# Performance work log

Measured on AMD Instinct MI355X. Metric: run time of the kernel, lower is better.

The kernel has to match this reference:

```python
import jax, jax.numpy as jnp
import numpy as np

B, C, H, W = 8, 256, 128, 128


def setup_inputs() -> dict:
    key = jax.random.key(0)
    ks = jax.random.split(key, 4)
    scale = 1.0 / np.sqrt(C)
    x = jax.random.normal(ks[0], (B, C, H, W), dtype=jnp.float32)
    Wq = jax.random.normal(ks[1], (C, C), dtype=jnp.float32) * scale
    Wk = jax.random.normal(ks[2], (C, C), dtype=jnp.float32) * scale
    Wv = jax.random.normal(ks[3], (C, C), dtype=jnp.float32) * scale
    bq = jnp.zeros((C,), dtype=jnp.float32)
    bk = jnp.zeros((C,), dtype=jnp.float32)
    bv = jnp.zeros((C,), dtype=jnp.float32)
    gamma = jnp.zeros((1,), dtype=jnp.float32)
    return {"x": x, "Wq": Wq, "bq": bq, "Wk": Wk, "bk": bk, "Wv": Wv, "bv": bv, "gamma": gamma}


def reference(x, Wq, bq, Wk, bk, Wv, bv, gamma):
    b, c, h, w = x.shape
    n = h * w
    xf = x.reshape(b, c, n)  # [B, C, N]
    # 1x1 convs == per-pixel linear over channels (W is [out, in])
    q = jnp.einsum('bcn,oc->bon', xf, Wq) + bq[None, :, None]  # [B, C, N]
    k = jnp.einsum('bcn,oc->bon', xf, Wk) + bk[None, :, None]
    v = jnp.einsum('bcn,oc->bon', xf, Wv) + bv[None, :, None]
    # energy[b,i,j] = sum_n k[b,i,n] * q[b,j,n]  -> [B, C, C]
    energy = jnp.einsum('bin,bjn->bij', k, q)
    attention = jax.nn.softmax(energy, axis=-1)
    # out[b,j,n] = sum_i attention[b,i,j] * v[b,i,n]  (attention^T @ v)
    out = jnp.einsum('bij,bin->bjn', attention, v)
    out = out.reshape(b, c, h, w)
    return gamma[0] * out + x
```

## Files before the change

kernel.cpp:

```cpp
#include <hip/hip_runtime.h>

#define C_DIM 256
#define N_DIM 16384
#define NBATCH 8

typedef __bf16 bf16x4 __attribute__((ext_vector_type(4)));
typedef __bf16 bf16x8 __attribute__((ext_vector_type(8)));
typedef float  f32x4  __attribute__((ext_vector_type(4)));

#define OFF_G   0x000000u
#define OFF_SP  0x200000u
#define OFF_EK  0x240000u
#define OFF_EQ  0x242000u
#define OFF_D   0x244000u
#define OFF_T1  0x250000u
#define OFF_E   0x450000u
#define OFF_P   0x650000u
#define OFF_GP  0x1000000u

__device__ __forceinline__ unsigned sw_off(int row, int kbyte) {
  return (unsigned)(row * 128 + (kbyte ^ ((((row >> 2) ^ row) & 7) << 4)));
}
__device__ __forceinline__ float f4g(const float4& v, int i) {
  return reinterpret_cast<const float*>(&v)[i];
}

__global__ __launch_bounds__(512, 2) void k1_syrk(const float* __restrict__ x,
                                                  __bf16* __restrict__ Gp,
                                                  float* __restrict__ sp,
                                                  const float* __restrict__ gm) {
  if (gm[0] == 0.0f) return;
  __shared__ __align__(16) char Alds[256 * 128];
  __shared__ float s_lds[256];
  const int b = blockIdx.y;
  const float* xb = x + (size_t)b * C_DIM * N_DIM;
  const int tid = threadIdx.x, lane = tid & 63, wave = tid >> 6;
  const int wm = wave >> 1, wn = wave & 1;
  const int k4 = tid & 15, rowt = tid >> 4;
  const size_t nbase = (size_t)blockIdx.x * 512;
  f32x4 acc[4][8] = {};
  float spart[8];
#pragma unroll
  for (int p = 0; p < 8; ++p) spart[p] = 0.f;

  float4 va[8];
  {
#pragma unroll
    for (int p = 0; p < 8; ++p)
      va[p] = *(const float4*)&xb[(size_t)(rowt + p * 32) * N_DIM + nbase + 4 * k4];
  }

  for (int ks = 0; ks < 8; ++ks) {
    __syncthreads();
#pragma unroll
    for (int p = 0; p < 8; ++p) {
      const int row = rowt + p * 32;
      spart[p] += va[p].x + va[p].y + va[p].z + va[p].w;
      bf16x4 ha = { (__bf16)va[p].x, (__bf16)va[p].y, (__bf16)va[p].z, (__bf16)va[p].w };
      *(bf16x4*)(Alds + sw_off(row, 8 * k4)) = ha;
    }
    __syncthreads();
    if (ks < 7) {
      const size_t n0 = nbase + (size_t)(ks + 1) * 64 + 4 * k4;
#pragma unroll
      for (int p = 0; p < 8; ++p)
        va[p] = *(const float4*)&xb[(size_t)(rowt + p * 32) * N_DIM + n0];
    }
#pragma unroll
    for (int kk = 0; kk < 2; ++kk) {
      bf16x8 af[4], bfr[8];
      const int kbyte = (kk * 32 + (lane >> 4) * 8) * 2;
#pragma unroll
      for (int mi = 0; mi < 4; ++mi)
        af[mi] = *(const bf16x8*)(Alds + sw_off(wm * 64 + mi * 16 + (lane & 15), kbyte));
#pragma unroll
      for (int ni = 0; ni < 8; ++ni)
        bfr[ni] = *(const bf16x8*)(Alds + sw_off(wn * 128 + ni * 16 + (lane & 15), kbyte));
#pragma unroll
      for (int mi = 0; mi < 4; ++mi)
#pragma unroll
        for (int ni = 0; ni < 8; ++ni)
          acc[mi][ni] = __builtin_amdgcn_mfma_f32_16x16x32_bf16(af[mi], bfr[ni], acc[mi][ni], 0, 0, 0);
    }
  }

  __bf16* Gout = Gp + ((size_t)blockIdx.x * NBATCH + b) * 65536;
#pragma unroll
  for (int mi = 0; mi < 4; ++mi)
#pragma unroll
    for (int ni = 0; ni < 8; ++ni)
#pragma unroll
      for (int r = 0; r < 4; ++r) {
        const int gr = wm * 64 + mi * 16 + (lane >> 4) * 4 + r;
        const int gc = wn * 128 + ni * 16 + (lane & 15);
        Gout[gr * 256 + gc] = (__bf16)acc[mi][ni][r];
      }

  __syncthreads();
  if (tid < 256) s_lds[tid] = 0.f;
  __syncthreads();
#pragma unroll
  for (int p = 0; p < 8; ++p) atomicAdd(&s_lds[rowt + p * 32], spart[p]);
  __syncthreads();
  if (tid < 256) sp[((size_t)blockIdx.x * NBATCH + b) * 256 + tid] = s_lds[tid];
}

__global__ __launch_bounds__(256) void k1_reduce(const __bf16* __restrict__ Gp,
                                                 float* __restrict__ G,
                                                 const float* __restrict__ Wq,
                                                 const float* __restrict__ Wk,
                                                 const float* __restrict__ sp,
                                                 float* __restrict__ ek,
                                                 float* __restrict__ eq,
                                                 const float* __restrict__ gm) {
  if (gm[0] == 0.0f) return;
  if (blockIdx.x >= 256) {
    __shared__ float s_sh[256];
    const int b = blockIdx.x - 256;
    const int t = threadIdx.x;
    float sv = 0.f;
#pragma unroll
    for (int p = 0; p < 32; ++p) sv += sp[((size_t)p * NBATCH + b) * 256 + t];
    s_sh[t] = sv;
    __syncthreads();
    float aK = 0.f, aQ = 0.f;
#pragma unroll 8
    for (int i = 0; i < 256; i += 4) {
      const float4 wk4 = *(const float4*)&Wk[t * 256 + i];
      const float4 wq4 = *(const float4*)&Wq[t * 256 + i];
      const float4 svv = *(const float4*)&s_sh[i];
      aK += wk4.x * svv.x + wk4.y * svv.y + wk4.z * svv.z + wk4.w * svv.w;
      aQ += wq4.x * svv.x + wq4.y * svv.y + wq4.z * svv.z + wq4.w * svv.w;
    }
    ek[b * 256 + t] = aK;
    eq[b * 256 + t] = aQ;
    return;
  }
  const size_t idx = ((size_t)blockIdx.x * 256 + threadIdx.x) * 8;
  float acc[8] = {};
#pragma unroll
  for (int p = 0; p < 32; ++p) {
    const bf16x8 v = *(const bf16x8*)&Gp[(size_t)p * NBATCH * 65536 + idx];
#pragma unroll
    for (int j = 0; j < 8; ++j) acc[j] += (float)v[j];
  }
  f32x4 lo = { acc[0], acc[1], acc[2], acc[3] };
  f32x4 hi = { acc[4], acc[5], acc[6], acc[7] };
  *(f32x4*)&G[idx]     = lo;
  *(f32x4*)&G[idx + 4] = hi;
}

__global__ __launch_bounds__(256) void k2_nt(const float* __restrict__ Ag, int abatch,
                                             const float* __restrict__ Bg, int bbatch,
                                             float* __restrict__ Cg,
                                             const float* __restrict__ ek,
                                             const float* __restrict__ bq,
                                             const float* __restrict__ bk,
                                             const float* __restrict__ eq,
                                             float Nf, int bias,
                                             const float* __restrict__ gm) {
  if (gm[0] == 0.0f) return;
  const int b = blockIdx.z;
  const float* A = Ag + (abatch ? (size_t)b * 65536 : 0);
  const float* B = Bg + (bbatch ? (size_t)b * 65536 : 0);
  float* Cb = Cg + (size_t)b * 65536;
  const int i0 = blockIdx.y * 64 + 4 * (threadIdx.x >> 4);
  const int c0 = blockIdx.x * 64 + 4 * (threadIdx.x & 15);
  float acc[4][4] = {};
  for (int k = 0; k < 256; k += 4) {
    float4 av[4], bv4[4];
#pragma unroll
    for (int r = 0; r < 4; ++r) av[r] = *(const float4*)&A[(size_t)(i0 + r) * 256 + k];
#pragma unroll
    for (int s2 = 0; s2 < 4; ++s2) bv4[s2] = *(const float4*)&B[(size_t)(c0 + s2) * 256 + k];
#pragma unroll
    for (int r = 0; r < 4; ++r)
#pragma unroll
      for (int s2 = 0; s2 < 4; ++s2)
        acc[r][s2] += av[r].x * bv4[s2].x + av[r].y * bv4[s2].y +
                      av[r].z * bv4[s2].z + av[r].w * bv4[s2].w;
  }
#pragma unroll
  for (int r = 0; r < 4; ++r)
#pragma unroll
    for (int s2 = 0; s2 < 4; ++s2) {
      const int i = i0 + r, j = c0 + s2;
      float v = acc[r][s2];
      if (bias) v += ek[b * 256 + i] * bq[j] + bk[i] * (eq[b * 256 + j] + Nf * bq[j]);
      Cb[(size_t)i * 256 + j] = v;
    }
}

__global__ __launch_bounds__(256) void k2_softmax(float* __restrict__ E,
                                                  const float* __restrict__ gm) {
  if (gm[0] == 0.0f) return;
  const int gw = blockIdx.x * 4 + (threadIdx.x >> 6);
  const int b = gw >> 8, i = gw & 255;
  const int lane = threadIdx.x & 63;
  float* row = E + (size_t)b * 65536 + (size_t)i * 256;
  float4 v = *(const float4*)&row[lane * 4];
  float m = fmaxf(fmaxf(v.x, v.y), fmaxf(v.z, v.w));
  for (int o = 32; o > 0; o >>= 1) m = fmaxf(m, __shfl_xor(m, o));
  v.x = __expf(v.x - m); v.y = __expf(v.y - m);
  v.z = __expf(v.z - m); v.w = __expf(v.w - m);
  float sum = v.x + v.y + v.z + v.w;
  for (int o = 32; o > 0; o >>= 1) sum += __shfl_xor(sum, o);
  const float inv = 1.0f / sum;
  v.x *= inv; v.y *= inv; v.z *= inv; v.w *= inv;
  *(float4*)&row[lane * 4] = v;
}

__global__ __launch_bounds__(256) void k2_pprime(const float* __restrict__ Att,
                                                 const float* __restrict__ Wv,
                                                 const float* __restrict__ bv,
                                                 const float* __restrict__ gm,
                                                 __bf16* __restrict__ P,
                                                 float* __restrict__ dv) {
  if (gm[0] == 0.0f) return;
  const int b = blockIdx.z;
  const float* Ab = Att + (size_t)b * 65536;
  const int j0 = blockIdx.y * 64 + 4 * (threadIdx.x >> 4);
  const int c0 = blockIdx.x * 64 + 4 * (threadIdx.x & 15);
  float acc[4][4] = {};
#pragma unroll 4
  for (int i = 0; i < 256; ++i) {
    float4 av = *(const float4*)&Ab[(size_t)i * 256 + j0];
    float4 wv = *(const float4*)&Wv[(size_t)i * 256 + c0];
#pragma unroll
    for (int r = 0; r < 4; ++r) {
      const float a = f4g(av, r);
#pragma unroll
      for (int s2 = 0; s2 < 4; ++s2) acc[r][s2] += a * f4g(wv, s2);
    }
  }
  const float g = gm[0];
  __bf16* Pb = P + (size_t)b * 65536;
#pragma unroll
  for (int r = 0; r < 4; ++r)
#pragma unroll
    for (int s2 = 0; s2 < 4; ++s2) {
      const float v = g * acc[r][s2] + ((j0 + r) == (c0 + s2) ? 1.f : 0.f);
      Pb[(size_t)(j0 + r) * 256 + c0 + s2] = (__bf16)v;
    }
  if (blockIdx.x == 0 && threadIdx.x < 64) {
    const int j = blockIdx.y * 64 + threadIdx.x;
    float a = 0.f;
    for (int i = 0; i < 256; ++i) a += Ab[(size_t)i * 256 + j] * bv[i];
    dv[b * 256 + j] = g * a;
  }
}

__global__ __launch_bounds__(512) void k3_out(const float* __restrict__ x,
                                              const __bf16* __restrict__ P,
                                              const float* __restrict__ dvec,
                                              const float* __restrict__ gm,
                                              float* __restrict__ out) {
  const int b = blockIdx.y, nt = blockIdx.x;
  const float* xb = x + (size_t)b * C_DIM * N_DIM;
  float* ob = out + (size_t)b * C_DIM * N_DIM;
  const int tid = threadIdx.x;
  const int n0 = nt * 128;

  if (gm[0] == 0.0f) {
#pragma unroll
    for (int it = 0; it < 16; ++it) {
      const int idx = it * 512 + tid;
      const int row = idx >> 5;
      const int c4  = (idx & 31) * 4;
      *(float4*)&ob[(size_t)row * N_DIM + n0 + c4] =
          *(const float4*)&xb[(size_t)row * N_DIM + n0 + c4];
    }
    return;
  }

  __shared__ __align__(16) char Alds[256 * 128];
  __shared__ __align__(16) char Blds[128 * 128];
  const __bf16* Pb = P + (size_t)b * 65536;
  const int lane = tid & 63, wave = tid >> 6;
  const int jw = wave >> 1, nw = wave & 1;
  const int k4 = tid & 15, rowt = tid >> 4;
  const int nq = tid & 31, cq = tid >> 5;
  f32x4 acc[4][4] = {};

  bf16x4 pa[8];
  float4 xv[4];
  {
#pragma unroll
    for (int p = 0; p < 8; ++p)
      pa[p] = *(const bf16x4*)&Pb[(size_t)(rowt + p * 32) * 256 + 4 * k4];
    const int cc = 4 * cq;
#pragma unroll
    for (int r = 0; r < 4; ++r)
      xv[r] = *(const float4*)&xb[(size_t)(cc + r) * N_DIM + n0 + 4 * nq];
  }

  for (int ks = 0; ks < 4; ++ks) {
    __syncthreads();
#pragma unroll
    for (int p = 0; p < 8; ++p)
      *(bf16x4*)(Alds + sw_off(rowt + p * 32, 8 * k4)) = pa[p];
    {
      const int cb = (4 * cq) * 2;
#pragma unroll
      for (int i = 0; i < 4; ++i) {
        bf16x4 t = { (__bf16)f4g(xv[0], i), (__bf16)f4g(xv[1], i),
                     (__bf16)f4g(xv[2], i), (__bf16)f4g(xv[3], i) };
        *(bf16x4*)(Blds + sw_off(4 * nq + i, cb)) = t;
      }
    }
    __syncthreads();
    if (ks < 3) {
      const int c0 = (ks + 1) * 64;
#pragma unroll
      for (int p = 0; p < 8; ++p)
        pa[p] = *(const bf16x4*)&Pb[(size_t)(rowt + p * 32) * 256 + c0 + 4 * k4];
      const int cc = c0 + 4 * cq;
#pragma unroll
      for (int r = 0; r < 4; ++r)
        xv[r] = *(const float4*)&xb[(size_t)(cc + r) * N_DIM + n0 + 4 * nq];
    }
#pragma unroll
    for (int kk = 0; kk < 2; ++kk) {
      bf16x8 af[4], bfr[4];
      const int kbyte = (kk * 32 + (lane >> 4) * 8) * 2;
#pragma unroll
      for (int mi = 0; mi < 4; ++mi)
        af[mi] = *(const bf16x8*)(Alds + sw_off(jw * 64 + mi * 16 + (lane & 15), kbyte));
#pragma unroll
      for (int ni = 0; ni < 4; ++ni)
        bfr[ni] = *(const bf16x8*)(Blds + sw_off(nw * 64 + ni * 16 + (lane & 15), kbyte));
#pragma unroll
      for (int mi = 0; mi < 4; ++mi)
#pragma unroll
        for (int ni = 0; ni < 4; ++ni)
          acc[mi][ni] = __builtin_amdgcn_mfma_f32_16x16x32_bf16(af[mi], bfr[ni], acc[mi][ni], 0, 0, 0);
    }
  }

#pragma unroll
  for (int mi = 0; mi < 4; ++mi)
#pragma unroll
    for (int ni = 0; ni < 4; ++ni)
#pragma unroll
      for (int r = 0; r < 4; ++r) {
        const int j = jw * 64 + mi * 16 + (lane >> 4) * 4 + r;
        const int n = n0 + nw * 64 + ni * 16 + (lane & 15);
        ob[(size_t)j * N_DIM + n] = acc[mi][ni][r] + dvec[b * 256 + j];
      }
}

extern "C" void kernel_launch(void* const* d_in, const int* in_sizes, int n_in,
                              void* d_out, int out_size, void* d_ws, size_t ws_size,
                              hipStream_t stream) {
  const float* x  = (const float*)d_in[0];
  const float* Wq = (const float*)d_in[1];
  const float* bq = (const float*)d_in[2];
  const float* Wk = (const float*)d_in[3];
  const float* bk = (const float*)d_in[4];
  const float* Wv = (const float*)d_in[5];
  const float* bv = (const float*)d_in[6];
  const float* gm = (const float*)d_in[7];
  float* out = (float*)d_out;
  char* ws = (char*)d_ws;
  float* G  = (float*)(ws + OFF_G);
  float* sp = (float*)(ws + OFF_SP);
  float* ek = (float*)(ws + OFF_EK);
  float* eq = (float*)(ws + OFF_EQ);
  float* dv = (float*)(ws + OFF_D);
  float* T1 = (float*)(ws + OFF_T1);
  float* E  = (float*)(ws + OFF_E);
  __bf16* P = (__bf16*)(ws + OFF_P);
  __bf16* Gp = (__bf16*)(ws + OFF_GP);


  k1_syrk<<<dim3(32, 8), dim3(512), 0, stream>>>(x, Gp, sp, gm);
  k1_reduce<<<dim3(264), dim3(256), 0, stream>>>(Gp, G, Wq, Wk, sp, ek, eq, gm);
  k2_nt<<<dim3(4, 4, 8), dim3(256), 0, stream>>>(Wk, 0, G, 1, T1,
                                                 nullptr, nullptr, nullptr, nullptr, 0.f, 0, gm);
  k2_nt<<<dim3(4, 4, 8), dim3(256), 0, stream>>>(T1, 1, Wq, 0, E,
                                                 ek, bq, bk, eq, (float)N_DIM, 1, gm);
  k2_softmax<<<dim3(512), dim3(256), 0, stream>>>(E, gm);
  k2_pprime<<<dim3(4, 4, 8), dim3(256), 0, stream>>>(E, Wv, bv, gm, P, dv);
  k3_out<<<dim3(128, 8), dim3(512), 0, stream>>>(x, P, dv, gm, out);
}
```

Measured before the change: 57.88 us.

## Fuse middle attention kernels into one per-batch kernel; streamline gamma-zero copy

Replaces the reduce, two small GEMMs, softmax and P-prime kernels with a single kernel that runs one 512-thread block per batch. Energy, softmax and projection now run in sequence inside that block, with workspace round-trips and block-wide syncs between stages. The intent is to cut kernel launches and inter-kernel gaps, since these stages exit early when gamma is zero. The gamma-zero path of the output kernel now copies contiguous flat chunks with nontemporal stores. The trade-off is that with nonzero gamma the fused middle stage runs on only 8 blocks, so it has far less parallelism.

```diff
diff --git a/kernel.cpp b/kernel.cpp
--- a/kernel.cpp
+++ b/kernel.cpp
@@ -8,10 +8,7 @@
 typedef __bf16 bf16x8 __attribute__((ext_vector_type(8)));
 typedef float  f32x4  __attribute__((ext_vector_type(4)));
 
-#define OFF_G   0x000000u
 #define OFF_SP  0x200000u
-#define OFF_EK  0x240000u
-#define OFF_EQ  0x242000u
 #define OFF_D   0x244000u
 #define OFF_T1  0x250000u
 #define OFF_E   0x450000u
@@ -105,148 +102,160 @@
   if (tid < 256) sp[((size_t)blockIdx.x * NBATCH + b) * 256 + tid] = s_lds[tid];
 }
 
-__global__ __launch_bounds__(256) void k1_reduce(const __bf16* __restrict__ Gp,
-                                                 float* __restrict__ G,
-                                                 const float* __restrict__ Wq,
-                                                 const float* __restrict__ Wk,
-                                                 const float* __restrict__ sp,
-                                                 float* __restrict__ ek,
-                                                 float* __restrict__ eq,
-                                                 const float* __restrict__ gm) {
-  if (gm[0] == 0.0f) return;
-  if (blockIdx.x >= 256) {
-    __shared__ float s_sh[256];
-    const int b = blockIdx.x - 256;
-    const int t = threadIdx.x;
-    float sv = 0.f;
-#pragma unroll
-    for (int p = 0; p < 32; ++p) sv += sp[((size_t)p * NBATCH + b) * 256 + t];
-    s_sh[t] = sv;
-    __syncthreads();
-    float aK = 0.f, aQ = 0.f;
-#pragma unroll 8
-    for (int i = 0; i < 256; i += 4) {
-      const float4 wk4 = *(const float4*)&Wk[t * 256 + i];
-      const float4 wq4 = *(const float4*)&Wq[t * 256 + i];
-      const float4 svv = *(const float4*)&s_sh[i];
-      aK += wk4.x * svv.x + wk4.y * svv.y + wk4.z * svv.z + wk4.w * svv.w;
-      aQ += wq4.x * svv.x + wq4.y * svv.y + wq4.z * svv.z + wq4.w * svv.w;
-    }
-    ek[b * 256 + t] = aK;
-    eq[b * 256 + t] = aQ;
-    return;
-  }
-  const size_t idx = ((size_t)blockIdx.x * 256 + threadIdx.x) * 8;
-  float acc[8] = {};
-#pragma unroll
-  for (int p = 0; p < 32; ++p) {
-    const bf16x8 v = *(const bf16x8*)&Gp[(size_t)p * NBATCH * 65536 + idx];
-#pragma unroll
-    for (int j = 0; j < 8; ++j) acc[j] += (float)v[j];
-  }
-  f32x4 lo = { acc[0], acc[1], acc[2], acc[3] };
-  f32x4 hi = { acc[4], acc[5], acc[6], acc[7] };
-  *(f32x4*)&G[idx]     = lo;
-  *(f32x4*)&G[idx + 4] = hi;
-}
-
-__global__ __launch_bounds__(256) void k2_nt(const float* __restrict__ Ag, int abatch,
-                                             const float* __restrict__ Bg, int bbatch,
-                                             float* __restrict__ Cg,
-                                             const float* __restrict__ ek,
+__global__ __launch_bounds__(512) void k_mid(const __bf16* __restrict__ Gp,
+                                             const float* __restrict__ Wq,
+                                             const float* __restrict__ Wk,
+                                             const float* __restrict__ Wv,
+                                             const float* __restrict__ sp,
                                              const float* __restrict__ bq,
                                              const float* __restrict__ bk,
-                                             const float* __restrict__ eq,
-                                             float Nf, int bias,
-                                             const float* __restrict__ gm) {
+                                             const float* __restrict__ bv,
+                                             const float* __restrict__ gm,
+                                             float* __restrict__ Gbuf,
+                                             float* __restrict__ T1buf,
+                                             __bf16* __restrict__ P,
+                                             float* __restrict__ dv) {
   if (gm[0] == 0.0f) return;
-  const int b = blockIdx.z;
-  const float* A = Ag + (abatch ? (size_t)b * 65536 : 0);
-  const float* B = Bg + (bbatch ? (size_t)b * 65536 : 0);
-  float* Cb = Cg + (size_t)b * 65536;
-  const int i0 = blockIdx.y * 64 + 4 * (threadIdx.x >> 4);
-  const int c0 = blockIdx.x * 64 + 4 * (threadIdx.x & 15);
-  float acc[4][4] = {};
-  for (int k = 0; k < 256; k += 4) {
-    float4 av[4], bv4[4];
-#pragma unroll
-    for (int r = 0; r < 4; ++r) av[r] = *(const float4*)&A[(size_t)(i0 + r) * 256 + k];
-#pragma unroll
-    for (int s2 = 0; s2 < 4; ++s2) bv4[s2] = *(const float4*)&B[(size_t)(c0 + s2) * 256 + k];
-#pragma unroll
-    for (int r = 0; r < 4; ++r)
-#pragma unroll
-      for (int s2 = 0; s2 < 4; ++s2)
-        acc[r][s2] += av[r].x * bv4[s2].x + av[r].y * bv4[s2].y +
-                      av[r].z * bv4[s2].z + av[r].w * bv4[s2].w;
-  }
-#pragma unroll
-  for (int r = 0; r < 4; ++r)
-#pragma unroll
-    for (int s2 = 0; s2 < 4; ++s2) {
-      const int i = i0 + r, j = c0 + s2;
-      float v = acc[r][s2];
-      if (bias) v += ek[b * 256 + i] * bq[j] + bk[i] * (eq[b * 256 + j] + Nf * bq[j]);
-      Cb[(size_t)i * 256 + j] = v;
-    }
-}
-
-__global__ __launch_bounds__(256) void k2_softmax(float* __restrict__ E,
-                                                  const float* __restrict__ gm) {
-  if (gm[0] == 0.0f) return;
-  const int gw = blockIdx.x * 4 + (threadIdx.x >> 6);
-  const int b = gw >> 8, i = gw & 255;
-  const int lane = threadIdx.x & 63;
-  float* row = E + (size_t)b * 65536 + (size_t)i * 256;
-  float4 v = *(const float4*)&row[lane * 4];
-  float m = fmaxf(fmaxf(v.x, v.y), fmaxf(v.z, v.w));
-  for (int o = 32; o > 0; o >>= 1) m = fmaxf(m, __shfl_xor(m, o));
-  v.x = __expf(v.x - m); v.y = __expf(v.y - m);
-  v.z = __expf(v.z - m); v.w = __expf(v.w - m);
-  float sum = v.x + v.y + v.z + v.w;
-  for (int o = 32; o > 0; o >>= 1) sum += __shfl_xor(sum, o);
-  const float inv = 1.0f / sum;
-  v.x *= inv; v.y *= inv; v.z *= inv; v.w *= inv;
-  *(float4*)&row[lane * 4] = v;
-}
-
-__global__ __launch_bounds__(256) void k2_pprime(const float* __restrict__ Att,
-                                                 const float* __restrict__ Wv,
-                                                 const float* __restrict__ bv,
-                                                 const float* __restrict__ gm,
-                                                 __bf16* __restrict__ P,
-                                                 float* __restrict__ dv) {
-  if (gm[0] == 0.0f) return;
-  const int b = blockIdx.z;
-  const float* Ab = Att + (size_t)b * 65536;
-  const int j0 = blockIdx.y * 64 + 4 * (threadIdx.x >> 4);
-  const int c0 = blockIdx.x * 64 + 4 * (threadIdx.x & 15);
-  float acc[4][4] = {};
-#pragma unroll 4
-  for (int i = 0; i < 256; ++i) {
-    float4 av = *(const float4*)&Ab[(size_t)i * 256 + j0];
-    float4 wv = *(const float4*)&Wv[(size_t)i * 256 + c0];
-#pragma unroll
-    for (int r = 0; r < 4; ++r) {
-      const float a = f4g(av, r);
-#pragma unroll
-      for (int s2 = 0; s2 < 4; ++s2) acc[r][s2] += a * f4g(wv, s2);
-    }
-  }
+  const int b = blockIdx.x, tid = threadIdx.x;
+  __shared__ float s_sh[256], ek_sh[256], eq_sh[256];
+  float* Gb  = Gbuf  + (size_t)b * 65536;
+  float* T1b = T1buf + (size_t)b * 65536;
+
+  if (tid < 256) {
+    float sv = 0.f;
+    for (int p = 0; p < 32; ++p) sv += sp[(size_t)(p * NBATCH + b) * 256 + tid];
+    s_sh[tid] = sv;
+  }
+  __syncthreads();
+  {
+    const int t = tid & 255;
+    const float* W = (tid < 256) ? Wk : Wq;
+    float a = 0.f;
+    for (int i = 0; i < 256; i += 4) {
+      const float4 w4 = *(const float4*)&W[(size_t)t * 256 + i];
+      const float4 s4 = *(const float4*)&s_sh[i];
+      a += w4.x * s4.x + w4.y * s4.y + w4.z * s4.z + w4.w * s4.w;
+    }
+    if (tid < 256) ek_sh[t] = a; else eq_sh[t] = a;
+  }
+
+  for (int u = 0; u < 16; ++u) {
+    const int c8 = (u * 512 + tid) * 8;
+    float acc[8] = {};
+    for (int p = 0; p < 32; ++p) {
+      const bf16x8 v = *(const bf16x8*)&Gp[(size_t)(p * NBATCH + b) * 65536 + c8];
+#pragma unroll
+      for (int j = 0; j < 8; ++j) acc[j] += (float)v[j];
+    }
+    f32x4 lo = { acc[0], acc[1], acc[2], acc[3] };
+    f32x4 hi = { acc[4], acc[5], acc[6], acc[7] };
+    *(f32x4*)&Gb[c8] = lo; *(f32x4*)&Gb[c8 + 4] = hi;
+  }
+  __syncthreads();
+
+  const int jv = 4 * (tid & 15);
+  const int iv = 4 * (tid >> 4);
+
+  for (int ib = 0; ib < 2; ++ib)
+    for (int jb = 0; jb < 4; ++jb) {
+      const int i0 = ib * 128 + iv, j0 = jb * 64 + jv;
+      float acc[4][4] = {};
+      for (int k = 0; k < 256; k += 4) {
+        float4 a4[4], g4[4];
+#pragma unroll
+        for (int r = 0; r < 4; ++r) a4[r] = *(const float4*)&Wk[(size_t)(i0 + r) * 256 + k];
+#pragma unroll
+        for (int kk = 0; kk < 4; ++kk) g4[kk] = *(const float4*)&Gb[(size_t)(k + kk) * 256 + j0];
+#pragma unroll
+        for (int r = 0; r < 4; ++r)
+#pragma unroll
+          for (int kk = 0; kk < 4; ++kk) {
+            const float av = f4g(a4[r], kk);
+#pragma unroll
+            for (int c = 0; c < 4; ++c) acc[r][c] += av * f4g(g4[kk], c);
+          }
+      }
+#pragma unroll
+      for (int r = 0; r < 4; ++r) {
+        f32x4 o = { acc[r][0], acc[r][1], acc[r][2], acc[r][3] };
+        *(f32x4*)&T1b[(size_t)(i0 + r) * 256 + j0] = o;
+      }
+    }
+  __syncthreads();
+
+  const float Nf = (float)N_DIM;
+  for (int ib = 0; ib < 2; ++ib)
+    for (int jb = 0; jb < 4; ++jb) {
+      const int i0 = ib * 128 + iv, j0 = jb * 64 + jv;
+      float acc[4][4] = {};
+      for (int k = 0; k < 256; k += 4) {
+        float4 a4[4], w4[4];
+#pragma unroll
+        for (int r = 0; r < 4; ++r) a4[r] = *(const float4*)&T1b[(size_t)(i0 + r) * 256 + k];
+#pragma unroll
+        for (int c = 0; c < 4; ++c) w4[c] = *(const float4*)&Wq[(size_t)(j0 + c) * 256 + k];
+#pragma unroll
+        for (int r = 0; r < 4; ++r)
+#pragma unroll
+          for (int c = 0; c < 4; ++c)
+            acc[r][c] += f4g(a4[r],0) * f4g(w4[c],0) + f4g(a4[r],1) * f4g(w4[c],1)
+                       + f4g(a4[r],2) * f4g(w4[c],2) + f4g(a4[r],3) * f4g(w4[c],3);
+      }
+#pragma unroll
+      for (int r = 0; r < 4; ++r)
+#pragma unroll
+        for (int c = 0; c < 4; ++c) {
+          const int i = i0 + r, j = j0 + c;
+          Gb[(size_t)i * 256 + j] = acc[r][c] + ek_sh[i] * bq[j] + bk[i] * (eq_sh[j] + Nf * bq[j]);
+        }
+    }
+  __syncthreads();
+
+  {
+    const int wv2 = tid >> 6, lane = tid & 63;
+    for (int rr = 0; rr < 32; ++rr) {
+      const int row = wv2 * 32 + rr;
+      float4 v = *(const float4*)&Gb[(size_t)row * 256 + lane * 4];
+      float m = fmaxf(fmaxf(v.x, v.y), fmaxf(v.z, v.w));
+      for (int o = 32; o > 0; o >>= 1) m = fmaxf(m, __shfl_xor(m, o));
+      v.x = __expf(v.x - m); v.y = __expf(v.y - m);
+      v.z = __expf(v.z - m); v.w = __expf(v.w - m);
+      float sum = v.x + v.y + v.z + v.w;
+      for (int o = 32; o > 0; o >>= 1) sum += __shfl_xor(sum, o);
+      const float inv = 1.0f / sum;
+      v.x *= inv; v.y *= inv; v.z *= inv; v.w *= inv;
+      *(float4*)&Gb[(size_t)row * 256 + lane * 4] = v;
+    }
+  }
+  __syncthreads();
+
   const float g = gm[0];
   __bf16* Pb = P + (size_t)b * 65536;
-#pragma unroll
-  for (int r = 0; r < 4; ++r)
-#pragma unroll
-    for (int s2 = 0; s2 < 4; ++s2) {
-      const float v = g * acc[r][s2] + ((j0 + r) == (c0 + s2) ? 1.f : 0.f);
-      Pb[(size_t)(j0 + r) * 256 + c0 + s2] = (__bf16)v;
-    }
-  if (blockIdx.x == 0 && threadIdx.x < 64) {
-    const int j = blockIdx.y * 64 + threadIdx.x;
+  for (int jb = 0; jb < 2; ++jb)
+    for (int cb = 0; cb < 4; ++cb) {
+      const int j0 = jb * 128 + iv, c0 = cb * 64 + jv;
+      float acc[4][4] = {};
+      for (int i = 0; i < 256; ++i) {
+        const float4 av  = *(const float4*)&Gb[(size_t)i * 256 + j0];
+        const float4 wv4 = *(const float4*)&Wv[(size_t)i * 256 + c0];
+#pragma unroll
+        for (int r = 0; r < 4; ++r) {
+          const float a = f4g(av, r);
+#pragma unroll
+          for (int c = 0; c < 4; ++c) acc[r][c] += a * f4g(wv4, c);
+        }
+      }
+#pragma unroll
+      for (int r = 0; r < 4; ++r)
+#pragma unroll
+        for (int c = 0; c < 4; ++c)
+          Pb[(size_t)(j0 + r) * 256 + c0 + c] =
+              (__bf16)(g * acc[r][c] + ((j0 + r) == (c0 + c) ? 1.f : 0.f));
+    }
+  if (tid < 256) {
     float a = 0.f;
-    for (int i = 0; i < 256; ++i) a += Ab[(size_t)i * 256 + j] * bv[i];
-    dv[b * 256 + j] = g * a;
+    for (int i = 0; i < 256; ++i) a += Gb[(size_t)i * 256 + tid] * bv[i];
+    dv[b * 256 + tid] = g * a;
   }
 }
 
@@ -255,31 +264,32 @@
                                               const float* __restrict__ dvec,
                                               const float* __restrict__ gm,
                                               float* __restrict__ out) {
+  const int tid = threadIdx.x;
+
+  if (gm[0] == 0.0f) {
+    const size_t base = (size_t)(blockIdx.y * gridDim.x + blockIdx.x) * 8192;
+    const f32x4* xi = (const f32x4*)x;
+    f32x4* oo = (f32x4*)out;
+#pragma unroll
+    for (int it = 0; it < 16; ++it) {
+      const size_t idx = base + (size_t)it * 512 + tid;
+      const f32x4 v = xi[idx];
+      __builtin_nontemporal_store(v, &oo[idx]);
+    }
+    return;
+  }
+
+  __shared__ __align__(16) char Alds[256 * 128];
+  __shared__ __align__(16) char Blds[128 * 128];
   const int b = blockIdx.y, nt = blockIdx.x;
   const float* xb = x + (size_t)b * C_DIM * N_DIM;
   float* ob = out + (size_t)b * C_DIM * N_DIM;
-  const int tid = threadIdx.x;
-  const int n0 = nt * 128;
-
-  if (gm[0] == 0.0f) {
-#pragma unroll
-    for (int it = 0; it < 16; ++it) {
-      const int idx = it * 512 + tid;
-      const int row = idx >> 5;
-      const int c4  = (idx & 31) * 4;
-      *(float4*)&ob[(size_t)row * N_DIM + n0 + c4] =
-          *(const float4*)&xb[(size_t)row * N_DIM + n0 + c4];
-    }
-    return;
-  }
-
-  __shared__ __align__(16) char Alds[256 * 128];
-  __shared__ __align__(16) char Blds[128 * 128];
   const __bf16* Pb = P + (size_t)b * 65536;
   const int lane = tid & 63, wave = tid >> 6;
   const int jw = wave >> 1, nw = wave & 1;
   const int k4 = tid & 15, rowt = tid >> 4;
   const int nq = tid & 31, cq = tid >> 5;
+  const int n0 = nt * 128;
   f32x4 acc[4][4] = {};
 
   bf16x4 pa[8];
@@ -362,24 +372,15 @@
   const float* gm = (const float*)d_in[7];
   float* out = (float*)d_out;
   char* ws = (char*)d_ws;
-  float* G  = (float*)(ws + OFF_G);
   float* sp = (float*)(ws + OFF_SP);
-  float* ek = (float*)(ws + OFF_EK);
-  float* eq = (float*)(ws + OFF_EQ);
   float* dv = (float*)(ws + OFF_D);
   float* T1 = (float*)(ws + OFF_T1);
-  float* E  = (float*)(ws + OFF_E);
+  float* Gb = (float*)(ws + OFF_E);
   __bf16* P = (__bf16*)(ws + OFF_P);
   __bf16* Gp = (__bf16*)(ws + OFF_GP);
 
-
   k1_syrk<<<dim3(32, 8), dim3(512), 0, stream>>>(x, Gp, sp, gm);
-  k1_reduce<<<dim3(264), dim3(256), 0, stream>>>(Gp, G, Wq, Wk, sp, ek, eq, gm);
-  k2_nt<<<dim3(4, 4, 8), dim3(256), 0, stream>>>(Wk, 0, G, 1, T1,
-                                                 nullptr, nullptr, nullptr, nullptr, 0.f, 0, gm);
-  k2_nt<<<dim3(4, 4, 8), dim3(256), 0, stream>>>(T1, 1, Wq, 0, E,
-                                                 ek, bq, bk, eq, (float)N_DIM, 1, gm);
-  k2_softmax<<<dim3(512), dim3(256), 0, stream>>>(E, gm);
-  k2_pprime<<<dim3(4, 4, 8), dim3(256), 0, stream>>>(E, Wv, bv, gm, P, dv);
+  k_mid<<<dim3(8), dim3(512), 0, stream>>>(Gp, Wq, Wk, Wv, sp, bq, bk, bv, gm,
+                                           Gb, T1, P, dv);
   k3_out<<<dim3(128, 8), dim3(512), 0, stream>>>(x, P, dv, gm, out);
 }
```

Result: faster. 51.78 us (-10.5%).
